# Performance work log

Measured on AMD Instinct MI355X. Metric: run time of the kernel, lower is better.

The kernel has to match this reference:

```python
import jax, jax.numpy as jnp
import numpy as np

C = 2048      # num_features
G = 4         # groups
L = C // G    # per-group channel count
EPS = 1e-4
N = 16384     # batch (flattened N*H*W with H=W=1)


def setup_inputs() -> dict:
    key = jax.random.key(0)
    k1, k2, k3 = jax.random.split(key, 3)
    x = jax.random.normal(k1, (C, N), dtype=jnp.float32)
    weight = jax.random.uniform(k2, (C, 1), dtype=jnp.float32)   # reset_parameters: uniform_()
    bias = jax.random.normal(k3, (C, 1), dtype=jnp.float32) * 0.05
    return {"x": x, "weight": weight, "bias": bias}


def reference(x, weight, bias):
    # Training-path ZCA whitening (the high-headroom path of ZCANormSVDPI).
    # Per group: cov = xg xg^T / N + eps*I ; truncated ZCA via eigendecomposition.
    # PowerIterationOnce.forward is identity (returns v_k), and with exact
    # eigenvectors the Rayleigh quotient lambda_ij equals the eigenvalue e_j,
    # so subspace = sum_{j < counter} v_j v_j^T / sqrt(e_j), where counter is
    # the first j with cumulative-energy ratio >= 1-eps or e_j <= eps.
    mu = jnp.mean(x, axis=1, keepdims=True)            # (C,1)
    xc = x - mu
    xg = xc.reshape(G, L, N)                           # per-group centered data
    eye = jnp.eye(L, dtype=x.dtype)
    cov = jnp.einsum('gin,gjn->gij', xg, xg) / N + EPS * eye  # (G,L,L)

    # symmetric PSD: eigh == svd of the original code; sort descending
    e, v = jnp.linalg.eigh(cov)                        # ascending
    e = e[:, ::-1]                                     # (G,L) descending
    v = v[:, :, ::-1]                                  # (G,L,L) columns = eigenvectors

    ratio = jnp.cumsum(e, axis=1) / jnp.sum(e, axis=1, keepdims=True)
    brk = (ratio >= 1.0 - EPS) | (e <= EPS)            # break condition at index j
    keep = jnp.cumprod(1 - brk.astype(jnp.int32), axis=1).astype(bool)  # j kept iff no break at k<=j

    e_safe = jnp.where(keep, e, 1.0)
    scale = jnp.where(keep, jax.lax.rsqrt(e_safe), 0.0)  # 1/sqrt(lambda_j), masked
    subspace = jnp.einsum('gij,gj,gkj->gik', v, scale, v)  # (G,L,L) whitening matrices

    xgr = jnp.einsum('gik,gkn->gin', subspace, xg).reshape(C, N)
    return xgr * weight + bias                         # (C,N), same layout as input
```

## Files before the change

### kernel.cpp

```cpp
#include <hip/hip_runtime.h>
#include <stdint.h>
#include <math.h>

#define C_DIM 2048
#define N_DIM 16384
#define L_DIM 512
#define G_NUM 4
#define EPSV 1e-4f

#define CHEB_D 8
#define NSQ 14
#define ALPHA_S 1.55f
#define CB_A 0.50
#define CB_B 1.55

typedef __attribute__((ext_vector_type(8))) short bf16x8;
typedef __attribute__((ext_vector_type(4))) float f32x4;

static __device__ __forceinline__ unsigned short f2bf(float f) {
  union { float f; unsigned int u; } v; v.f = f;
  unsigned int u = v.u;
  unsigned int r = (u + 0x7FFFu + ((u >> 16) & 1u)) >> 16;
  return (unsigned short)r;
}
static __device__ __forceinline__ float bf2f(unsigned short h) {
  union { unsigned int u; float f; } v; v.u = ((unsigned int)h) << 16;
  return v.f;
}

__global__ __launch_bounds__(256) void k1_mean_split(
    const float* __restrict__ x, unsigned short* __restrict__ hi,
    unsigned short* __restrict__ lo, float* __restrict__ mu) {
  int c = blockIdx.x;
  const float* row = x + (size_t)c * N_DIM;
  unsigned short* hrow = hi + (size_t)c * N_DIM;
  unsigned short* lrow = lo + (size_t)c * N_DIM;
  float s = 0.f;
  for (int i = threadIdx.x * 4; i < N_DIM; i += 1024) {
    float4 v = *(const float4*)(row + i);
    s += (v.x + v.y) + (v.z + v.w);
    unsigned short h0 = f2bf(v.x), h1 = f2bf(v.y), h2 = f2bf(v.z), h3 = f2bf(v.w);
    ushort4 hh; hh.x = h0; hh.y = h1; hh.z = h2; hh.w = h3;
    *(ushort4*)(hrow + i) = hh;
    ushort4 ll;
    ll.x = f2bf(v.x - bf2f(h0)); ll.y = f2bf(v.y - bf2f(h1));
    ll.z = f2bf(v.z - bf2f(h2)); ll.w = f2bf(v.w - bf2f(h3));
    *(ushort4*)(lrow + i) = ll;
  }
#pragma unroll
  for (int off = 32; off > 0; off >>= 1) s += __shfl_down(s, off);
  __shared__ float red[4];
  if ((threadIdx.x & 63) == 0) red[threadIdx.x >> 6] = s;
  __syncthreads();
  if (threadIdx.x == 0) mu[c] = (red[0] + red[1] + red[2] + red[3]) * (1.f / N_DIM);
}

__global__ __launch_bounds__(256) void k2_cov(
    const unsigned short* __restrict__ hi, const unsigned short* __restrict__ lo,
    float* __restrict__ S) {
  int bid = blockIdx.x;
  int kc = bid >> 6; int rem = bid & 63; int g = rem >> 4; int t = rem & 15;
  int ti = t >> 2, tj = t & 3;
  int lane = threadIdx.x & 63, w = threadIdx.x >> 6;
  int wi = w >> 1, wj = w & 1;
  int l15 = lane & 15, lg = lane >> 4;
  int r0 = g * L_DIM + ti * 128 + wi * 64;
  int c0 = g * L_DIM + tj * 128 + wj * 64;
  f32x4 zz = {0.f, 0.f, 0.f, 0.f};
  f32x4 acc[4][4];
#pragma unroll
  for (int a = 0; a < 4; a++)
#pragma unroll
    for (int b = 0; b < 4; b++) acc[a][b] = zz;
  size_t kb = (size_t)kc * 2048 + (size_t)lg * 8;
  for (int k = 0; k < 2048; k += 32) {
    bf16x8 ah[4], al[4], bh[4], bl[4];
#pragma unroll
    for (int a = 0; a < 4; a++) {
      size_t o = (size_t)(r0 + a * 16 + l15) * N_DIM + kb + k;
      ah[a] = *(const bf16x8*)(hi + o);
      al[a] = *(const bf16x8*)(lo + o);
    }
#pragma unroll
    for (int b = 0; b < 4; b++) {
      size_t o = (size_t)(c0 + b * 16 + l15) * N_DIM + kb + k;
      bh[b] = *(const bf16x8*)(hi + o);
      bl[b] = *(const bf16x8*)(lo + o);
    }
#pragma unroll
    for (int a = 0; a < 4; a++)
#pragma unroll
      for (int b = 0; b < 4; b++) {
        acc[a][b] = __builtin_amdgcn_mfma_f32_16x16x32_bf16(ah[a], bh[b], acc[a][b], 0, 0, 0);
        acc[a][b] = __builtin_amdgcn_mfma_f32_16x16x32_bf16(ah[a], bl[b], acc[a][b], 0, 0, 0);
        acc[a][b] = __builtin_amdgcn_mfma_f32_16x16x32_bf16(al[a], bh[b], acc[a][b], 0, 0, 0);
      }
  }
  float* Sg = S + (size_t)g * L_DIM * L_DIM;
#pragma unroll
  for (int a = 0; a < 4; a++) {
    int rl = ti * 128 + wi * 64 + a * 16 + 4 * lg;
#pragma unroll
    for (int b = 0; b < 4; b++) {
      int cl = tj * 128 + wj * 64 + b * 16 + l15;
#pragma unroll
      for (int i = 0; i < 4; i++)
        atomicAdd(&Sg[(size_t)(rl + i) * L_DIM + cl], acc[a][b][i]);
    }
  }
}

__global__ __launch_bounds__(256) void k3_assemble(
    float* __restrict__ S, const float* __restrict__ mu, float c0h, float c1,
    float* __restrict__ Pacc,
    unsigned short* __restrict__ Mhi, unsigned short* __restrict__ Mlo,
    unsigned short* __restrict__ B0hi, unsigned short* __restrict__ B0lo,
    unsigned short* __restrict__ T0hi, unsigned short* __restrict__ T0lo,
    float* __restrict__ trc) {
  size_t idx = (size_t)blockIdx.x * 256 + threadIdx.x;
  int g = (int)(idx >> 18); int r = (int)((idx >> 9) & 511); int cc = (int)(idx & 511);
  float diag = (r == cc) ? 1.f : 0.f;
  float s = S[idx] * (1.f / N_DIM) - mu[g * 512 + r] * mu[g * 512 + cc] + diag * EPSV;
  S[idx] = s;
  float m = (2.f * s - diag * (float)(CB_A + CB_B)) * (float)(1.0 / (CB_B - CB_A));
  unsigned short mh = f2bf(m); Mhi[idx] = mh; Mlo[idx] = f2bf(m - bf2f(mh));
  float b0 = diag * ALPHA_S - s;
  unsigned short bh = f2bf(b0); B0hi[idx] = bh; B0lo[idx] = f2bf(b0 - bf2f(bh));
  Pacc[idx] = c0h * diag + c1 * m;
  T0hi[idx] = (r == cc) ? (unsigned short)0x3F80 : (unsigned short)0;
  T0lo[idx] = 0;
  if (r == cc) atomicAdd(&trc[g], b0);
}

__global__ __launch_bounds__(256) void k4_chain(
    const unsigned short* __restrict__ Ahi, const unsigned short* __restrict__ Alo,
    const unsigned short* __restrict__ Bhi, const unsigned short* __restrict__ Blo,
    unsigned short* __restrict__ Dhi, unsigned short* __restrict__ Dlo,
    int mode,
    const unsigned short* __restrict__ Phi, const unsigned short* __restrict__ Plo,
    float coeff, float* __restrict__ Pacc,
    const float* __restrict__ tr_in, float* __restrict__ tr_out) {
  int bid = blockIdx.x;
  int g = bid >> 6; int t = bid & 63; int ti = t >> 3, tj = t & 7;
  int lane = threadIdx.x & 63, w = threadIdx.x >> 6;
  int wi = w >> 1, wj = w & 1;
  int l15 = lane & 15, lg = lane >> 4;
  int r0 = ti * 64 + wi * 32, c0 = tj * 64 + wj * 32;
  size_t gof = (size_t)g * (L_DIM * L_DIM);
  const unsigned short* Ah = Ahi + gof; const unsigned short* Al = Alo + gof;
  const unsigned short* Bh = Bhi + gof; const unsigned short* Bl = Blo + gof;
  f32x4 zz = {0.f, 0.f, 0.f, 0.f};
  f32x4 acc[2][2];
  acc[0][0] = zz; acc[0][1] = zz; acc[1][0] = zz; acc[1][1] = zz;
  for (int k = 0; k < 512; k += 32) {
    int ko = k + lg * 8;
    bf16x8 ah[2], al2[2], bh[2], bl2[2];
#pragma unroll
    for (int a = 0; a < 2; a++) {
      size_t o = (size_t)(r0 + a * 16 + l15) * 512 + ko;
      ah[a] = *(const bf16x8*)(Ah + o); al2[a] = *(const bf16x8*)(Al + o);
    }
#pragma unroll
    for (int b = 0; b < 2; b++) {
      size_t o = (size_t)(c0 + b * 16 + l15) * 512 + ko;
      bh[b] = *(const bf16x8*)(Bh + o); bl2[b] = *(const bf16x8*)(Bl + o);
    }
#pragma unroll
    for (int a = 0; a < 2; a++)
#pragma unroll
      for (int b = 0; b < 2; b++) {
        acc[a][b] = __builtin_amdgcn_mfma_f32_16x16x32_bf16(ah[a], bh[b], acc[a][b], 0, 0, 0);
        acc[a][b] = __builtin_amdgcn_mfma_f32_16x16x32_bf16(ah[a], bl2[b], acc[a][b], 0, 0, 0);
        acc[a][b] = __builtin_amdgcn_mfma_f32_16x16x32_bf16(al2[a], bh[b], acc[a][b], 0, 0, 0);
      }
  }
  float scale = 1.f;
  if (mode == 1) { float th = tr_in[g] * (1.f / 512.f); scale = 1.f / (th * th); }
#pragma unroll
  for (int a = 0; a < 2; a++) {
    int rr = r0 + a * 16 + 4 * lg;
#pragma unroll
    for (int b = 0; b < 2; b++) {
      int cc = c0 + b * 16 + l15;
#pragma unroll
      for (int i = 0; i < 4; i++) {
        size_t di = gof + (size_t)(rr + i) * 512 + cc;
        float d = acc[a][b][i];
        if (mode == 0) {
          d = 2.f * d - (bf2f(Phi[di]) + bf2f(Plo[di]));
          unsigned short dh = f2bf(d);
          Dhi[di] = dh; Dlo[di] = f2bf(d - bf2f(dh));
          Pacc[di] += coeff * d;
        } else {
          d *= scale;
          unsigned short dh = f2bf(d);
          Dhi[di] = dh; Dlo[di] = f2bf(d - bf2f(dh));
          if (rr + i == cc) atomicAdd(&tr_out[g], d);
        }
      }
    }
  }
}

__global__ __launch_bounds__(256) void k5_extract(
    const unsigned short* __restrict__ Bhi, const unsigned short* __restrict__ Blo,
    const float* __restrict__ S, float* __restrict__ vbuf, float* __restrict__ smin) {
  int g = blockIdx.x; int tid = threadIdx.x;
  size_t gof = (size_t)g * (512 * 512);
  __shared__ float sv[256]; __shared__ int si[256];
  __shared__ float vrow[512];
  float best = -1e30f; int bj = 0;
  for (int j = tid; j < 512; j += 256) {
    size_t di = gof + (size_t)j * 512 + j;
    float dv = bf2f(Bhi[di]) + bf2f(Blo[di]);
    if (dv > best) { best = dv; bj = j; }
  }
  sv[tid] = best; si[tid] = bj; __syncthreads();
  for (int s2 = 128; s2 > 0; s2 >>= 1) {
    if (tid < s2 && sv[tid + s2] > sv[tid]) { sv[tid] = sv[tid + s2]; si[tid] = si[tid + s2]; }
    __syncthreads();
  }
  int jm = si[0]; __syncthreads();
  float nl = 0.f;
  for (int j = tid; j < 512; j += 256) {
    size_t ri = gof + (size_t)jm * 512 + j;
    float vv = bf2f(Bhi[ri]) + bf2f(Blo[ri]);
    vrow[j] = vv; nl += vv * vv;
  }
  sv[tid] = nl; __syncthreads();
  for (int s2 = 128; s2 > 0; s2 >>= 1) { if (tid < s2) sv[tid] += sv[tid + s2]; __syncthreads(); }
  float inv = rsqrtf(sv[0]); __syncthreads();
  for (int j = tid; j < 512; j += 256) { vrow[j] *= inv; vbuf[g * 512 + j] = vrow[j]; }
  __syncthreads();
  float rloc = 0.f;
  for (int r = tid; r < 512; r += 256) {
    const float* Sr = S + gof + (size_t)r * 512;
    float u = 0.f;
    for (int j = 0; j < 512; j++) u += Sr[j] * vrow[j];
    rloc += u * vrow[r];
  }
  sv[tid] = rloc; __syncthreads();
  for (int s2 = 128; s2 > 0; s2 >>= 1) { if (tid < s2) sv[tid] += sv[tid + s2]; __syncthreads(); }
  if (tid == 0) smin[g] = rsqrtf(sv[0]);
}

__global__ __launch_bounds__(256) void k6_compose(
    const float* __restrict__ Pacc, const float* __restrict__ vbuf,
    const float* __restrict__ smin, const float* __restrict__ mu,
    unsigned short* __restrict__ Wbf, float* __restrict__ Wmu) {
  int c = blockIdx.x; int g = c >> 9; int r = c & 511;
  float vr = vbuf[g * 512 + r]; float sm = smin[g];
  float accv = 0.f;
  const float* Pr = Pacc + ((size_t)g * 512 + r) * 512;
  for (int j = threadIdx.x; j < 512; j += 256) {
    float wv = Pr[j] - sm * vr * vbuf[g * 512 + j];
    Wbf[(size_t)c * 512 + j] = f2bf(wv);
    accv += wv * mu[g * 512 + j];
  }
#pragma unroll
  for (int off = 32; off > 0; off >>= 1) accv += __shfl_down(accv, off);
  __shared__ float red[4];
  if ((threadIdx.x & 63) == 0) red[threadIdx.x >> 6] = accv;
  __syncthreads();
  if (threadIdx.x == 0) Wmu[c] = red[0] + red[1] + red[2] + red[3];
}

__global__ __launch_bounds__(256) void k7_apply(
    const unsigned short* __restrict__ Wbf, const unsigned short* __restrict__ hi,
    const float* __restrict__ Wmu, const float* __restrict__ weight,
    const float* __restrict__ bias, float* __restrict__ out) {
  int bid = blockIdx.x;
  int nt = bid & 63; int mt = (bid >> 6) & 3; int g = bid >> 8;
  int lane = threadIdx.x & 63, w = threadIdx.x >> 6;
  int l15 = lane & 15, lg = lane >> 4;
  int m0 = mt * 128;
  int n0 = nt * 256;
  __shared__ unsigned short ldsB[256][40];
  f32x4 zz = {0.f, 0.f, 0.f, 0.f};
  f32x4 acc[8][4];
#pragma unroll
  for (int a = 0; a < 8; a++)
#pragma unroll
    for (int b = 0; b < 4; b++) acc[a][b] = zz;
  const unsigned short* Wg = Wbf + ((size_t)g * 512 + m0) * 512;
  const unsigned short* hg = hi + (size_t)g * 512 * N_DIM;
  for (int k = 0; k < 512; k += 32) {
    __syncthreads();
    for (int v = threadIdx.x; v < 1024; v += 256) {
      int kl = v >> 5; int nv = v & 31;
      bf16x8 vv = *(const bf16x8*)(hg + (size_t)(k + kl) * N_DIM + n0 + nv * 8);
#pragma unroll
      for (int e = 0; e < 8; e++) ldsB[nv * 8 + e][kl] = ((unsigned short*)&vv)[e];
    }
    __syncthreads();
    bf16x8 afr[8], bfr[4];
#pragma unroll
    for (int a = 0; a < 8; a++)
      afr[a] = *(const bf16x8*)(Wg + (size_t)(a * 16 + l15) * 512 + k + lg * 8);
#pragma unroll
    for (int b = 0; b < 4; b++)
      bfr[b] = *(const bf16x8*)(&ldsB[w * 64 + b * 16 + l15][lg * 8]);
#pragma unroll
    for (int a = 0; a < 8; a++)
#pragma unroll
      for (int b = 0; b < 4; b++)
        acc[a][b] = __builtin_amdgcn_mfma_f32_16x16x32_bf16(afr[a], bfr[b], acc[a][b], 0, 0, 0);
  }
#pragma unroll
  for (int a = 0; a < 8; a++) {
#pragma unroll
    for (int i = 0; i < 4; i++) {
      int c = g * 512 + m0 + a * 16 + 4 * lg + i;
      float wm = Wmu[c], wt = weight[c], bs = bias[c];
      float* orow = out + (size_t)c * N_DIM + n0 + w * 64;
#pragma unroll
      for (int b = 0; b < 4; b++)
        orow[b * 16 + l15] = (acc[a][b][i] - wm) * wt + bs;
    }
  }
}

extern "C" void kernel_launch(void* const* d_in, const int* in_sizes, int n_in,
                              void* d_out, int out_size, void* d_ws, size_t ws_size,
                              hipStream_t stream) {
  (void)in_sizes; (void)n_in; (void)out_size; (void)ws_size;
  const float* x = (const float*)d_in[0];
  const float* weight = (const float*)d_in[1];
  const float* bias = (const float*)d_in[2];
  float* out = (float*)d_out;

  char* ws = (char*)d_ws;
  size_t off = 0;
  auto alloc = [&](size_t bytes) -> char* {
    char* p = ws + off; off += (bytes + 255) & ~(size_t)255; return p;
  };
  const size_t MAT = (size_t)G_NUM * L_DIM * L_DIM;
  unsigned short* hi  = (unsigned short*)alloc((size_t)C_DIM * N_DIM * 2);
  float* S            = (float*)alloc(MAT * 4);
  float* Pacc         = (float*)alloc(MAT * 4);
  unsigned short* Mhi = (unsigned short*)alloc(MAT * 2);
  unsigned short* Mlo = (unsigned short*)alloc(MAT * 2);
  unsigned short* B0hi= (unsigned short*)alloc(MAT * 2);
  unsigned short* B0lo= (unsigned short*)alloc(MAT * 2);
  unsigned short* T0hi= (unsigned short*)alloc(MAT * 2);
  unsigned short* T0lo= (unsigned short*)alloc(MAT * 2);
  unsigned short* TAhi= (unsigned short*)alloc(MAT * 2);
  unsigned short* TAlo= (unsigned short*)alloc(MAT * 2);
  unsigned short* TBhi= (unsigned short*)alloc(MAT * 2);
  unsigned short* TBlo= (unsigned short*)alloc(MAT * 2);
  unsigned short* Wbf = (unsigned short*)alloc(MAT * 2);
  float* mu   = (float*)alloc(C_DIM * 4);
  float* trc  = (float*)alloc(64 * 4);
  float* vbuf = (float*)alloc(G_NUM * L_DIM * 4);
  float* smin = (float*)alloc(16);
  float* Wmu  = (float*)alloc(C_DIM * 4);
  unsigned short* lo = (unsigned short*)d_out;

  double cc[CHEB_D + 1];
  for (int k = 0; k <= CHEB_D; k++) cc[k] = 0.0;
  const int mq = 256;
  for (int j = 0; j < mq; j++) {
    double th = M_PI * (j + 0.5) / mq;
    double xx = 0.5 * (CB_B + CB_A) + 0.5 * (CB_B - CB_A) * cos(th);
    double fv = 1.0 / sqrt(xx);
    for (int k = 0; k <= CHEB_D; k++) cc[k] += (2.0 / mq) * fv * cos(k * th);
  }

  hipMemsetAsync(S, 0, MAT * 4, stream);
  hipMemsetAsync(trc, 0, 64 * 4, stream);

  k1_mean_split<<<2048, 256, 0, stream>>>(x, hi, lo, mu);
  k2_cov<<<512, 256, 0, stream>>>(hi, lo, S);
  k3_assemble<<<4096, 256, 0, stream>>>(S, mu, (float)(cc[0] * 0.5), (float)cc[1],
                                        Pacc, Mhi, Mlo, B0hi, B0lo, T0hi, T0lo, trc);

  {
    struct Step { const unsigned short *bh, *bl, *ph, *pl; unsigned short *dh, *dl; float cf; };
    Step st[7] = {
      { Mhi,  Mlo,  T0hi, T0lo, TAhi, TAlo, (float)cc[2] },
      { TAhi, TAlo, Mhi,  Mlo,  TBhi, TBlo, (float)cc[3] },
      { TBhi, TBlo, TAhi, TAlo, T0hi, T0lo, (float)cc[4] },
      { T0hi, T0lo, TBhi, TBlo, TAhi, TAlo, (float)cc[5] },
      { TAhi, TAlo, T0hi, T0lo, TBhi, TBlo, (float)cc[6] },
      { TBhi, TBlo, TAhi, TAlo, T0hi, T0lo, (float)cc[7] },
      { T0hi, T0lo, TBhi, TBlo, TAhi, TAlo, (float)cc[8] },
    };
    for (int i = 0; i < 7; i++)
      k4_chain<<<256, 256, 0, stream>>>(Mhi, Mlo, st[i].bh, st[i].bl, st[i].dh, st[i].dl,
                                        0, st[i].ph, st[i].pl, st[i].cf, Pacc,
                                        (const float*)nullptr, (float*)nullptr);
  }

  {
    const unsigned short* inh = B0hi; const unsigned short* inl = B0lo;
    for (int s = 0; s < NSQ; s++) {
      unsigned short* oh = (s % 2 == 0) ? TAhi : TBhi;
      unsigned short* ol = (s % 2 == 0) ? TAlo : TBlo;
      k4_chain<<<256, 256, 0, stream>>>(inh, inl, inh, inl, oh, ol,
                                        1, (const unsigned short*)nullptr,
                                        (const unsigned short*)nullptr, 0.f, (float*)nullptr,
                                        trc + (size_t)s * 4, trc + (size_t)(s + 1) * 4);
      inh = oh; inl = ol;
    }
    k5_extract<<<4, 256, 0, stream>>>(inh, inl, S, vbuf, smin);
  }

  k6_compose<<<2048, 256, 0, stream>>>(Pacc, vbuf, smin, mu, Wbf, Wmu);
  k7_apply<<<1024, 256, 0, stream>>>(Wbf, hi, Wmu, weight, bias, out);
}
```

Before: 1.446 ms.

## Fuse Chebyshev and squaring chains, exploit covariance symmetry, transpose x for apply

The covariance kernel now computes only the upper-triangular tiles, and the assemble kernel mirrors them. Each Chebyshev step and power-squaring step are launched together in one kernel with the blocks split between them, and the squaring count drops by one. x is converted to a transposed bf16 copy so the apply GEMM can read both operands straight from global memory instead of going through an LDS transpose. The Rayleigh quotient moves into a parallel kernel, and weight and bias are folded into the composed matrix. The extra transpose pass and the shorter squaring chain change memory traffic and the accuracy margin.

```diff
diff --git a/kernel.cpp b/kernel.cpp
--- a/kernel.cpp
+++ b/kernel.cpp
@@ -9,7 +9,7 @@
 #define EPSV 1e-4f
 
 #define CHEB_D 8
-#define NSQ 14
+#define NSQ 13
 #define ALPHA_S 1.55f
 #define CB_A 0.50
 #define CB_B 1.55
@@ -58,9 +58,11 @@
 __global__ __launch_bounds__(256) void k2_cov(
     const unsigned short* __restrict__ hi, const unsigned short* __restrict__ lo,
     float* __restrict__ S) {
+  const int TI[10] = {0,0,0,0,1,1,1,2,2,3};
+  const int TJ[10] = {0,1,2,3,1,2,3,2,3,3};
   int bid = blockIdx.x;
-  int kc = bid >> 6; int rem = bid & 63; int g = rem >> 4; int t = rem & 15;
-  int ti = t >> 2, tj = t & 3;
+  int t = bid % 10; int g = (bid / 10) & 3; int kc = bid / 40;
+  int ti = TI[t], tj = TJ[t];
   int lane = threadIdx.x & 63, w = threadIdx.x >> 6;
   int wi = w >> 1, wj = w & 1;
   int l15 = lane & 15, lg = lane >> 4;
@@ -110,8 +112,52 @@
   }
 }
 
+__global__ __launch_bounds__(256) void t1_transpose(
+    const float* __restrict__ x, unsigned short* __restrict__ hiT) {
+  __shared__ unsigned short tile[64][72];
+  int bid = blockIdx.x;
+  int ct = bid >> 8;
+  int nt = bid & 255;
+  int c0 = ct * 64, n0 = nt * 64;
+  int t = threadIdx.x;
+  {
+    int r = t >> 2;
+    int cc = (t & 3) * 16;
+    const float* xp = x + (size_t)(c0 + r) * N_DIM + n0 + cc;
+    float4 v0 = *(const float4*)(xp + 0);
+    float4 v1 = *(const float4*)(xp + 4);
+    float4 v2 = *(const float4*)(xp + 8);
+    float4 v3 = *(const float4*)(xp + 12);
+    bf16x8 p0, p1;
+    ((unsigned short*)&p0)[0] = f2bf(v0.x); ((unsigned short*)&p0)[1] = f2bf(v0.y);
+    ((unsigned short*)&p0)[2] = f2bf(v0.z); ((unsigned short*)&p0)[3] = f2bf(v0.w);
+    ((unsigned short*)&p0)[4] = f2bf(v1.x); ((unsigned short*)&p0)[5] = f2bf(v1.y);
+    ((unsigned short*)&p0)[6] = f2bf(v1.z); ((unsigned short*)&p0)[7] = f2bf(v1.w);
+    ((unsigned short*)&p1)[0] = f2bf(v2.x); ((unsigned short*)&p1)[1] = f2bf(v2.y);
+    ((unsigned short*)&p1)[2] = f2bf(v2.z); ((unsigned short*)&p1)[3] = f2bf(v2.w);
+    ((unsigned short*)&p1)[4] = f2bf(v3.x); ((unsigned short*)&p1)[5] = f2bf(v3.y);
+    ((unsigned short*)&p1)[6] = f2bf(v3.z); ((unsigned short*)&p1)[7] = f2bf(v3.w);
+    *(bf16x8*)&tile[r][cc] = p0;
+    *(bf16x8*)&tile[r][cc + 8] = p1;
+  }
+  __syncthreads();
+  {
+    int n = t >> 2;
+    int ck = (t & 3) * 16;
+    bf16x8 o0, o1;
+#pragma unroll
+    for (int i = 0; i < 8; i++) ((unsigned short*)&o0)[i] = tile[ck + i][n];
+#pragma unroll
+    for (int i = 0; i < 8; i++) ((unsigned short*)&o1)[i] = tile[ck + 8 + i][n];
+    unsigned short* op = hiT + (size_t)(n0 + n) * C_DIM + c0 + ck;
+    *(bf16x8*)(op) = o0;
+    *(bf16x8*)(op + 8) = o1;
+  }
+}
+
 __global__ __launch_bounds__(256) void k3_assemble(
-    float* __restrict__ S, const float* __restrict__ mu, float c0h, float c1,
+    const float* __restrict__ Sraw, float* __restrict__ Scov,
+    const float* __restrict__ mu, float c0h, float c1,
     float* __restrict__ Pacc,
     unsigned short* __restrict__ Mhi, unsigned short* __restrict__ Mlo,
     unsigned short* __restrict__ B0hi, unsigned short* __restrict__ B0lo,
@@ -119,9 +165,11 @@
     float* __restrict__ trc) {
   size_t idx = (size_t)blockIdx.x * 256 + threadIdx.x;
   int g = (int)(idx >> 18); int r = (int)((idx >> 9) & 511); int cc = (int)(idx & 511);
+  int rl = r <= cc ? r : cc, ch = r <= cc ? cc : r;
   float diag = (r == cc) ? 1.f : 0.f;
-  float s = S[idx] * (1.f / N_DIM) - mu[g * 512 + r] * mu[g * 512 + cc] + diag * EPSV;
-  S[idx] = s;
+  float raw = Sraw[((size_t)g << 18) + ((size_t)rl << 9) + ch];
+  float s = raw * (1.f / N_DIM) - mu[g * 512 + r] * mu[g * 512 + cc] + diag * EPSV;
+  Scov[idx] = s;
   float m = (2.f * s - diag * (float)(CB_A + CB_B)) * (float)(1.0 / (CB_B - CB_A));
   unsigned short mh = f2bf(m); Mhi[idx] = mh; Mlo[idx] = f2bf(m - bf2f(mh));
   float b0 = diag * ALPHA_S - s;
@@ -132,50 +180,56 @@
   if (r == cc) atomicAdd(&trc[g], b0);
 }
 
-__global__ __launch_bounds__(256) void k4_chain(
-    const unsigned short* __restrict__ Ahi, const unsigned short* __restrict__ Alo,
-    const unsigned short* __restrict__ Bhi, const unsigned short* __restrict__ Blo,
-    unsigned short* __restrict__ Dhi, unsigned short* __restrict__ Dlo,
-    int mode,
-    const unsigned short* __restrict__ Phi, const unsigned short* __restrict__ Plo,
+__global__ __launch_bounds__(256) void k4_fused(
+    int cheb_blocks,
+    const unsigned short* __restrict__ Mh, const unsigned short* __restrict__ Ml,
+    const unsigned short* __restrict__ Bh, const unsigned short* __restrict__ Bl,
+    const unsigned short* __restrict__ Ph, const unsigned short* __restrict__ Pl,
+    unsigned short* __restrict__ Dh, unsigned short* __restrict__ Dl,
     float coeff, float* __restrict__ Pacc,
+    const unsigned short* __restrict__ Qh, const unsigned short* __restrict__ Ql,
+    unsigned short* __restrict__ Eh, unsigned short* __restrict__ El,
     const float* __restrict__ tr_in, float* __restrict__ tr_out) {
   int bid = blockIdx.x;
-  int g = bid >> 6; int t = bid & 63; int ti = t >> 3, tj = t & 7;
+  bool sqr = bid >= cheb_blocks;
+  int t6 = sqr ? bid - cheb_blocks : bid;
+  int g = t6 >> 6; int t = t6 & 63; int ti = t >> 3, tj = t & 7;
   int lane = threadIdx.x & 63, w = threadIdx.x >> 6;
   int wi = w >> 1, wj = w & 1;
   int l15 = lane & 15, lg = lane >> 4;
   int r0 = ti * 64 + wi * 32, c0 = tj * 64 + wj * 32;
   size_t gof = (size_t)g * (L_DIM * L_DIM);
-  const unsigned short* Ah = Ahi + gof; const unsigned short* Al = Alo + gof;
-  const unsigned short* Bh = Bhi + gof; const unsigned short* Bl = Blo + gof;
+  const unsigned short* Ah_ = (sqr ? Qh : Mh) + gof;
+  const unsigned short* Al_ = (sqr ? Ql : Ml) + gof;
+  const unsigned short* Bh_ = (sqr ? Qh : Bh) + gof;
+  const unsigned short* Bl_ = (sqr ? Ql : Bl) + gof;
   f32x4 zz = {0.f, 0.f, 0.f, 0.f};
   f32x4 acc[2][2];
   acc[0][0] = zz; acc[0][1] = zz; acc[1][0] = zz; acc[1][1] = zz;
   for (int k = 0; k < 512; k += 32) {
     int ko = k + lg * 8;
-    bf16x8 ah[2], al2[2], bh[2], bl2[2];
+    bf16x8 ah[2], al2[2], bh2[2], bl2[2];
 #pragma unroll
     for (int a = 0; a < 2; a++) {
       size_t o = (size_t)(r0 + a * 16 + l15) * 512 + ko;
-      ah[a] = *(const bf16x8*)(Ah + o); al2[a] = *(const bf16x8*)(Al + o);
+      ah[a] = *(const bf16x8*)(Ah_ + o); al2[a] = *(const bf16x8*)(Al_ + o);
     }
 #pragma unroll
     for (int b = 0; b < 2; b++) {
       size_t o = (size_t)(c0 + b * 16 + l15) * 512 + ko;
-      bh[b] = *(const bf16x8*)(Bh + o); bl2[b] = *(const bf16x8*)(Bl + o);
+      bh2[b] = *(const bf16x8*)(Bh_ + o); bl2[b] = *(const bf16x8*)(Bl_ + o);
     }
 #pragma unroll
     for (int a = 0; a < 2; a++)
 #pragma unroll
       for (int b = 0; b < 2; b++) {
-        acc[a][b] = __builtin_amdgcn_mfma_f32_16x16x32_bf16(ah[a], bh[b], acc[a][b], 0, 0, 0);
+        acc[a][b] = __builtin_amdgcn_mfma_f32_16x16x32_bf16(ah[a], bh2[b], acc[a][b], 0, 0, 0);
         acc[a][b] = __builtin_amdgcn_mfma_f32_16x16x32_bf16(ah[a], bl2[b], acc[a][b], 0, 0, 0);
-        acc[a][b] = __builtin_amdgcn_mfma_f32_16x16x32_bf16(al2[a], bh[b], acc[a][b], 0, 0, 0);
+        acc[a][b] = __builtin_amdgcn_mfma_f32_16x16x32_bf16(al2[a], bh2[b], acc[a][b], 0, 0, 0);
       }
   }
   float scale = 1.f;
-  if (mode == 1) { float th = tr_in[g] * (1.f / 512.f); scale = 1.f / (th * th); }
+  if (sqr) { float th = tr_in[g] * (1.f / 512.f); scale = 1.f / (th * th); }
 #pragma unroll
   for (int a = 0; a < 2; a++) {
     int rr = r0 + a * 16 + 4 * lg;
@@ -186,15 +240,15 @@
       for (int i = 0; i < 4; i++) {
         size_t di = gof + (size_t)(rr + i) * 512 + cc;
         float d = acc[a][b][i];
-        if (mode == 0) {
-          d = 2.f * d - (bf2f(Phi[di]) + bf2f(Plo[di]));
+        if (!sqr) {
+          d = 2.f * d - (bf2f(Ph[di]) + bf2f(Pl[di]));
           unsigned short dh = f2bf(d);
-          Dhi[di] = dh; Dlo[di] = f2bf(d - bf2f(dh));
+          Dh[di] = dh; Dl[di] = f2bf(d - bf2f(dh));
           Pacc[di] += coeff * d;
         } else {
           d *= scale;
           unsigned short dh = f2bf(d);
-          Dhi[di] = dh; Dlo[di] = f2bf(d - bf2f(dh));
+          Eh[di] = dh; El[di] = f2bf(d - bf2f(dh));
           if (rr + i == cc) atomicAdd(&tr_out[g], d);
         }
       }
@@ -202,13 +256,12 @@
   }
 }
 
-__global__ __launch_bounds__(256) void k5_extract(
+__global__ __launch_bounds__(256) void k5a_extract(
     const unsigned short* __restrict__ Bhi, const unsigned short* __restrict__ Blo,
-    const float* __restrict__ S, float* __restrict__ vbuf, float* __restrict__ smin) {
+    float* __restrict__ vbuf) {
   int g = blockIdx.x; int tid = threadIdx.x;
   size_t gof = (size_t)g * (512 * 512);
   __shared__ float sv[256]; __shared__ int si[256];
-  __shared__ float vrow[512];
   float best = -1e30f; int bj = 0;
   for (int j = tid; j < 512; j += 256) {
     size_t di = gof + (size_t)j * 512 + j;
@@ -222,6 +275,7 @@
   }
   int jm = si[0]; __syncthreads();
   float nl = 0.f;
+  __shared__ float vrow[512];
   for (int j = tid; j < 512; j += 256) {
     size_t ri = gof + (size_t)jm * 512 + j;
     float vv = bf2f(Bhi[ri]) + bf2f(Blo[ri]);
@@ -229,93 +283,95 @@
   }
   sv[tid] = nl; __syncthreads();
   for (int s2 = 128; s2 > 0; s2 >>= 1) { if (tid < s2) sv[tid] += sv[tid + s2]; __syncthreads(); }
-  float inv = rsqrtf(sv[0]); __syncthreads();
-  for (int j = tid; j < 512; j += 256) { vrow[j] *= inv; vbuf[g * 512 + j] = vrow[j]; }
-  __syncthreads();
-  float rloc = 0.f;
-  for (int r = tid; r < 512; r += 256) {
-    const float* Sr = S + gof + (size_t)r * 512;
-    float u = 0.f;
-    for (int j = 0; j < 512; j++) u += Sr[j] * vrow[j];
-    rloc += u * vrow[r];
-  }
-  sv[tid] = rloc; __syncthreads();
-  for (int s2 = 128; s2 > 0; s2 >>= 1) { if (tid < s2) sv[tid] += sv[tid + s2]; __syncthreads(); }
-  if (tid == 0) smin[g] = rsqrtf(sv[0]);
+  float inv = rsqrtf(sv[0]);
+  for (int j = tid; j < 512; j += 256) vbuf[g * 512 + j] = vrow[j] * inv;
+}
+
+__global__ __launch_bounds__(256) void k5b_rayleigh(
+    const float* __restrict__ Scov, const float* __restrict__ vbuf,
+    float* __restrict__ dot) {
+  int bid = blockIdx.x; int g = bid >> 4; int r0 = (bid & 15) * 32;
+  int t = threadIdx.x;
+  int r = r0 + (t >> 3); int c0 = (t & 7) * 64;
+  const float* Sr = Scov + ((size_t)g * 512 + r) * 512 + c0;
+  const float* vg = vbuf + g * 512;
+  float s = 0.f;
+#pragma unroll
+  for (int j = 0; j < 64; j += 4) {
+    float4 sv = *(const float4*)(Sr + j);
+    s += sv.x * vg[c0 + j] + sv.y * vg[c0 + j + 1] + sv.z * vg[c0 + j + 2] + sv.w * vg[c0 + j + 3];
+  }
+  s += __shfl_xor(s, 1); s += __shfl_xor(s, 2); s += __shfl_xor(s, 4);
+  if ((t & 7) == 0) atomicAdd(&dot[g], s * vg[r]);
 }
 
 __global__ __launch_bounds__(256) void k6_compose(
     const float* __restrict__ Pacc, const float* __restrict__ vbuf,
-    const float* __restrict__ smin, const float* __restrict__ mu,
-    unsigned short* __restrict__ Wbf, float* __restrict__ Wmu) {
+    const float* __restrict__ dot, const float* __restrict__ mu,
+    const float* __restrict__ weight, const float* __restrict__ bias,
+    unsigned short* __restrict__ Wbf, float* __restrict__ off) {
   int c = blockIdx.x; int g = c >> 9; int r = c & 511;
-  float vr = vbuf[g * 512 + r]; float sm = smin[g];
+  float vr = vbuf[g * 512 + r]; float sm = rsqrtf(dot[g]);
+  float wt = weight[c];
   float accv = 0.f;
   const float* Pr = Pacc + ((size_t)g * 512 + r) * 512;
   for (int j = threadIdx.x; j < 512; j += 256) {
-    float wv = Pr[j] - sm * vr * vbuf[g * 512 + j];
+    float wv = (Pr[j] - sm * vr * vbuf[g * 512 + j]) * wt;
     Wbf[(size_t)c * 512 + j] = f2bf(wv);
     accv += wv * mu[g * 512 + j];
   }
 #pragma unroll
-  for (int off = 32; off > 0; off >>= 1) accv += __shfl_down(accv, off);
+  for (int o2 = 32; o2 > 0; o2 >>= 1) accv += __shfl_down(accv, o2);
   __shared__ float red[4];
   if ((threadIdx.x & 63) == 0) red[threadIdx.x >> 6] = accv;
   __syncthreads();
-  if (threadIdx.x == 0) Wmu[c] = red[0] + red[1] + red[2] + red[3];
+  if (threadIdx.x == 0) off[c] = bias[c] - (red[0] + red[1] + red[2] + red[3]);
 }
 
 __global__ __launch_bounds__(256) void k7_apply(
-    const unsigned short* __restrict__ Wbf, const unsigned short* __restrict__ hi,
-    const float* __restrict__ Wmu, const float* __restrict__ weight,
-    const float* __restrict__ bias, float* __restrict__ out) {
-  int bid = blockIdx.x;
-  int nt = bid & 63; int mt = (bid >> 6) & 3; int g = bid >> 8;
+    const unsigned short* __restrict__ Wbf, const unsigned short* __restrict__ hiT,
+    const float* __restrict__ off, float* __restrict__ out) {
+  int bid0 = blockIdx.x;
+  int bid = (bid0 & 7) * 256 + (bid0 >> 3);
+  int mt = bid & 3; int nt = (bid >> 2) & 127; int g = bid >> 9;
   int lane = threadIdx.x & 63, w = threadIdx.x >> 6;
+  int wi = w >> 1, wj = w & 1;
   int l15 = lane & 15, lg = lane >> 4;
-  int m0 = mt * 128;
-  int n0 = nt * 256;
-  __shared__ unsigned short ldsB[256][40];
+  int mbase = mt * 128 + wi * 64;
+  int nbase = nt * 128 + wj * 64;
+  const unsigned short* Wg = Wbf + (size_t)(g * 512 + mbase) * 512;
+  const unsigned short* Hg = hiT + (size_t)nbase * C_DIM + g * 512;
   f32x4 zz = {0.f, 0.f, 0.f, 0.f};
-  f32x4 acc[8][4];
-#pragma unroll
-  for (int a = 0; a < 8; a++)
+  f32x4 acc[4][4];
+#pragma unroll
+  for (int a = 0; a < 4; a++)
 #pragma unroll
     for (int b = 0; b < 4; b++) acc[a][b] = zz;
-  const unsigned short* Wg = Wbf + ((size_t)g * 512 + m0) * 512;
-  const unsigned short* hg = hi + (size_t)g * 512 * N_DIM;
   for (int k = 0; k < 512; k += 32) {
-    __syncthreads();
-    for (int v = threadIdx.x; v < 1024; v += 256) {
-      int kl = v >> 5; int nv = v & 31;
-      bf16x8 vv = *(const bf16x8*)(hg + (size_t)(k + kl) * N_DIM + n0 + nv * 8);
-#pragma unroll
-      for (int e = 0; e < 8; e++) ldsB[nv * 8 + e][kl] = ((unsigned short*)&vv)[e];
-    }
-    __syncthreads();
-    bf16x8 afr[8], bfr[4];
-#pragma unroll
-    for (int a = 0; a < 8; a++)
-      afr[a] = *(const bf16x8*)(Wg + (size_t)(a * 16 + l15) * 512 + k + lg * 8);
+    int ko = k + lg * 8;
+    bf16x8 af[4], bf[4];
+#pragma unroll
+    for (int a = 0; a < 4; a++)
+      af[a] = *(const bf16x8*)(Wg + (size_t)(a * 16 + l15) * 512 + ko);
 #pragma unroll
     for (int b = 0; b < 4; b++)
-      bfr[b] = *(const bf16x8*)(&ldsB[w * 64 + b * 16 + l15][lg * 8]);
-#pragma unroll
-    for (int a = 0; a < 8; a++)
+      bf[b] = *(const bf16x8*)(Hg + (size_t)(b * 16 + l15) * C_DIM + ko);
+#pragma unroll
+    for (int a = 0; a < 4; a++)
 #pragma unroll
       for (int b = 0; b < 4; b++)
-        acc[a][b] = __builtin_amdgcn_mfma_f32_16x16x32_bf16(afr[a], bfr[b], acc[a][b], 0, 0, 0);
-  }
-#pragma unroll
-  for (int a = 0; a < 8; a++) {
+        acc[a][b] = __builtin_amdgcn_mfma_f32_16x16x32_bf16(af[a], bf[b], acc[a][b], 0, 0, 0);
+  }
+#pragma unroll
+  for (int a = 0; a < 4; a++) {
 #pragma unroll
     for (int i = 0; i < 4; i++) {
-      int c = g * 512 + m0 + a * 16 + 4 * lg + i;
-      float wm = Wmu[c], wt = weight[c], bs = bias[c];
-      float* orow = out + (size_t)c * N_DIM + n0 + w * 64;
+      int c = g * 512 + mbase + a * 16 + 4 * lg + i;
+      float ofc = off[c];
+      float* orow = out + (size_t)c * N_DIM + nbase;
 #pragma unroll
       for (int b = 0; b < 4; b++)
-        orow[b * 16 + l15] = (acc[a][b][i] - wm) * wt + bs;
+        orow[b * 16 + l15] = acc[a][b][i] + ofc;
     }
   }
 }
@@ -330,13 +386,14 @@
   float* out = (float*)d_out;
 
   char* ws = (char*)d_ws;
-  size_t off = 0;
+  size_t off_b = 0;
   auto alloc = [&](size_t bytes) -> char* {
-    char* p = ws + off; off += (bytes + 255) & ~(size_t)255; return p;
+    char* p = ws + off_b; off_b += (bytes + 255) & ~(size_t)255; return p;
   };
   const size_t MAT = (size_t)G_NUM * L_DIM * L_DIM;
   unsigned short* hi  = (unsigned short*)alloc((size_t)C_DIM * N_DIM * 2);
-  float* S            = (float*)alloc(MAT * 4);
+  float* Sraw         = (float*)alloc(MAT * 4);
+  float* Scov         = (float*)alloc(MAT * 4);
   float* Pacc         = (float*)alloc(MAT * 4);
   unsigned short* Mhi = (unsigned short*)alloc(MAT * 2);
   unsigned short* Mlo = (unsigned short*)alloc(MAT * 2);
@@ -348,12 +405,16 @@
   unsigned short* TAlo= (unsigned short*)alloc(MAT * 2);
   unsigned short* TBhi= (unsigned short*)alloc(MAT * 2);
   unsigned short* TBlo= (unsigned short*)alloc(MAT * 2);
+  unsigned short* SAhi= (unsigned short*)alloc(MAT * 2);
+  unsigned short* SAlo= (unsigned short*)alloc(MAT * 2);
+  unsigned short* SBhi= (unsigned short*)alloc(MAT * 2);
+  unsigned short* SBlo= (unsigned short*)alloc(MAT * 2);
   unsigned short* Wbf = (unsigned short*)alloc(MAT * 2);
   float* mu   = (float*)alloc(C_DIM * 4);
   float* trc  = (float*)alloc(64 * 4);
   float* vbuf = (float*)alloc(G_NUM * L_DIM * 4);
-  float* smin = (float*)alloc(16);
-  float* Wmu  = (float*)alloc(C_DIM * 4);
+  float* offv = (float*)alloc(C_DIM * 4);
+  float* dot  = trc + 56;
   unsigned short* lo = (unsigned short*)d_out;
 
   double cc[CHEB_D + 1];
@@ -366,12 +427,13 @@
     for (int k = 0; k <= CHEB_D; k++) cc[k] += (2.0 / mq) * fv * cos(k * th);
   }
 
-  hipMemsetAsync(S, 0, MAT * 4, stream);
+  hipMemsetAsync(Sraw, 0, MAT * 4, stream);
   hipMemsetAsync(trc, 0, 64 * 4, stream);
 
   k1_mean_split<<<2048, 256, 0, stream>>>(x, hi, lo, mu);
-  k2_cov<<<512, 256, 0, stream>>>(hi, lo, S);
-  k3_assemble<<<4096, 256, 0, stream>>>(S, mu, (float)(cc[0] * 0.5), (float)cc[1],
+  k2_cov<<<320, 256, 0, stream>>>(hi, lo, Sraw);
+  t1_transpose<<<8192, 256, 0, stream>>>(x, hi);
+  k3_assemble<<<4096, 256, 0, stream>>>(Sraw, Scov, mu, (float)(cc[0] * 0.5), (float)cc[1],
                                         Pacc, Mhi, Mlo, B0hi, B0lo, T0hi, T0lo, trc);
 
   {
@@ -385,26 +447,27 @@
       { TBhi, TBlo, TAhi, TAlo, T0hi, T0lo, (float)cc[7] },
       { T0hi, T0lo, TBhi, TBlo, TAhi, TAlo, (float)cc[8] },
     };
-    for (int i = 0; i < 7; i++)
-      k4_chain<<<256, 256, 0, stream>>>(Mhi, Mlo, st[i].bh, st[i].bl, st[i].dh, st[i].dl,
-                                        0, st[i].ph, st[i].pl, st[i].cf, Pacc,
-                                        (const float*)nullptr, (float*)nullptr);
-  }
-
-  {
-    const unsigned short* inh = B0hi; const unsigned short* inl = B0lo;
+    const unsigned short* qh = B0hi; const unsigned short* ql = B0lo;
     for (int s = 0; s < NSQ; s++) {
-      unsigned short* oh = (s % 2 == 0) ? TAhi : TBhi;
-      unsigned short* ol = (s % 2 == 0) ? TAlo : TBlo;
-      k4_chain<<<256, 256, 0, stream>>>(inh, inl, inh, inl, oh, ol,
-                                        1, (const unsigned short*)nullptr,
-                                        (const unsigned short*)nullptr, 0.f, (float*)nullptr,
-                                        trc + (size_t)s * 4, trc + (size_t)(s + 1) * 4);
-      inh = oh; inl = ol;
-    }
-    k5_extract<<<4, 256, 0, stream>>>(inh, inl, S, vbuf, smin);
-  }
-
-  k6_compose<<<2048, 256, 0, stream>>>(Pacc, vbuf, smin, mu, Wbf, Wmu);
-  k7_apply<<<1024, 256, 0, stream>>>(Wbf, hi, Wmu, weight, bias, out);
-}
+      unsigned short* eh = (s % 2 == 0) ? SAhi : SBhi;
+      unsigned short* el = (s % 2 == 0) ? SAlo : SBlo;
+      if (s < 7) {
+        k4_fused<<<512, 256, 0, stream>>>(256, Mhi, Mlo,
+                                          st[s].bh, st[s].bl, st[s].ph, st[s].pl,
+                                          st[s].dh, st[s].dl, st[s].cf, Pacc,
+                                          qh, ql, eh, el,
+                                          trc + (size_t)s * 4, trc + (size_t)(s + 1) * 4);
+      } else {
+        k4_fused<<<256, 256, 0, stream>>>(0, Mhi, Mlo,
+                                          Mhi, Mlo, Mhi, Mlo, TAhi, TAlo, 0.f, Pacc,
+                                          qh, ql, eh, el,
+                                          trc + (size_t)s * 4, trc + (size_t)(s + 1) * 4);
+      }
+      qh = eh; ql = el;
+    }
+    k5a_extract<<<4, 256, 0, stream>>>(SAhi, SAlo, vbuf);
+  }
+  k5b_rayleigh<<<64, 256, 0, stream>>>(Scov, vbuf, dot);
+  k6_compose<<<2048, 256, 0, stream>>>(Pacc, vbuf, dot, mu, weight, bias, Wbf, offv);
+  k7_apply<<<2048, 256, 0, stream>>>(Wbf, hi, offv, out);
+}
```

Result: faster. 1.157 ms (-20.0%).
